# Kernel optimization log

Hardware: AMD Instinct MI355X
Metric: run time of the kernel (lower is better)

The kernel has to match this reference:

```python
import jax, jax.numpy as jnp
import numpy as np

B, H, W, C = 32, 32, 32, 256


def setup_inputs() -> dict:
    key = jax.random.key(0)
    k1, k2 = jax.random.split(key)
    feats1 = jax.random.normal(k1, (B, H, W, C), dtype=jnp.float32)
    feats2 = jax.random.normal(k2, (B, H, W, C), dtype=jnp.float32)
    return {"feats1": feats1, "feats2": feats2}


def reference(feats1, feats2):
    # Training path of LocalFeatureLoss (trainflag=True)
    b, h, w, c = feats1.shape
    l = h * w
    q = feats1.reshape(b, l, c)  # queries: (B, l, C)
    p = feats2.reshape(b, l, c)  # preds:   (B, l, C)
    # M[b, a, j] = <p[b,a], q[b,j]>  == fm2 @ fm1.T per batch
    M = jnp.einsum('bac,bjc->baj', p, q)  # (B, l_pred, l_query)
    max1 = jnp.argmax(M, axis=1)  # (B, l_q): best pred index for each query token
    max2 = jnp.argmax(M, axis=2)  # (B, l_p): best query index for each pred token
    # mutual nearest-neighbor check: m[b, j] = max2[b, max1[b, j]]
    m = jnp.take_along_axis(max2, max1, axis=1)  # (B, l_q)
    valid = jnp.arange(l)[None, :] == m          # (B, l_q) bool
    # gather matched pred descriptors and compute per-pair similarity
    matched_p = jnp.take_along_axis(p, max1[..., None], axis=1)  # (B, l_q, C)
    sims = jnp.sum(q * matched_p, axis=-1)                        # (B, l_q)
    cnt = jnp.sum(valid, axis=1).astype(sims.dtype)               # (B,)
    # mean over mutual NN pairs (torch mean over idx1)
    similarity = jnp.sum(jnp.where(valid, sims, 0.0), axis=1) / jnp.maximum(cnt, 1.0)
    return similarity
```

## Files before the change

kernel.cpp:

```cpp
#include <hip/hip_runtime.h>
#include <hip/hip_bf16.h>

#define BATCH 32
#define L 1024
#define CD 256
#define BM 128
#define BN 128
#define BK 64
#define NRT (L / BM)
#define NCT (L / BN)

typedef __bf16 bf16x8 __attribute__((ext_vector_type(8)));
typedef __bf16 bf16x4 __attribute__((ext_vector_type(4)));
typedef float  f32x4  __attribute__((ext_vector_type(4)));

__device__ __forceinline__ unsigned int enc_f32(float f) {
    unsigned int u = __float_as_uint(f);
    return ((int)u < 0) ? ~u : (u | 0x80000000u);
}
__device__ __forceinline__ float dec_f32(unsigned int u) {
    u = (u & 0x80000000u) ? (u & 0x7FFFFFFFu) : ~u;
    return __uint_as_float(u);
}
__device__ __forceinline__ unsigned long long pmax(unsigned long long a, unsigned long long b) {
    return a > b ? a : b;
}
__device__ __forceinline__ bf16x4 cvt4(float4 v) {
    bf16x4 o;
    o[0] = (__bf16)v.x; o[1] = (__bf16)v.y; o[2] = (__bf16)v.z; o[3] = (__bf16)v.w;
    return o;
}

__device__ __forceinline__ void block_sync_lgkm() {
    asm volatile("s_waitcnt lgkmcnt(0)" ::: "memory");
    __builtin_amdgcn_s_barrier();
    asm volatile("" ::: "memory");
}

__global__ __launch_bounds__(512, 4) void mm_argmax_kernel(
    const float* __restrict__ qg,
    const float* __restrict__ pg,
    unsigned long long* __restrict__ colpart,
    unsigned long long* __restrict__ rowpart)
{
    __shared__ __bf16 sA[2][BM * BK];
    __shared__ __bf16 sB[2][BN * BK];
    __shared__ unsigned long long sRow[2][BM];
    __shared__ unsigned long long sCol[4][BN];

    const int tid = threadIdx.x;
    const int bid = blockIdx.x;
    const int b    = bid & 31;
    const int tile = bid >> 5;
    const int rt   = tile >> 3;
    const int ct   = tile & 7;
    const int row0 = rt * BM;
    const int col0 = ct * BN;

    const int lane = tid & 63;
    const int w    = tid >> 6;
    const int wm   = w >> 1;
    const int wn   = w & 1;
    const int quad = lane >> 4;
    const int l16  = lane & 15;

    const float* pA = pg + ((size_t)b * L + row0) * CD;
    const float* pB = qg + ((size_t)b * L + col0) * CD;

    const int sr = tid >> 4;
    const int sl = tid & 15;

    f32x4 acc[2][4];
    #pragma unroll
    for (int tm = 0; tm < 2; ++tm)
        #pragma unroll
        for (int tn = 0; tn < 4; ++tn) acc[tm][tn] = (f32x4){0.f, 0.f, 0.f, 0.f};

    float4 pfA[4], pfB[4];

    #define LOADS(k0)                                                          \
        _Pragma("unroll")                                                      \
        for (int p = 0; p < 4; ++p) {                                          \
            pfA[p] = *(const float4*)(pA + (size_t)(p * 32 + sr) * CD + (k0) + sl * 4); \
            pfB[p] = *(const float4*)(pB + (size_t)(p * 32 + sr) * CD + (k0) + sl * 4); \
        }

    #define STAGE(buf)                                                         \
        _Pragma("unroll")                                                      \
        for (int p = 0; p < 4; ++p) {                                          \
            const int row_ = p * 32 + sr;                                      \
            const int idx_ = row_ * BK + (((sl >> 1) ^ (row_ & 7)) << 3) + ((sl & 1) << 2); \
            *(bf16x4*)&sA[buf][idx_] = cvt4(pfA[p]);                           \
            *(bf16x4*)&sB[buf][idx_] = cvt4(pfB[p]);                           \
        }

    #define COMPUTE(buf)                                                       \
        __builtin_amdgcn_s_setprio(1);                                         \
        _Pragma("unroll")                                                      \
        for (int kk = 0; kk < 2; ++kk) {                                       \
            const int sw = ((kk * 4 + quad) ^ (l16 & 7)) << 3;                 \
            bf16x8 a0 = *(const bf16x8*)&sA[buf][(wm * 32      + l16) * BK + sw]; \
            bf16x8 a1 = *(const bf16x8*)&sA[buf][(wm * 32 + 16 + l16) * BK + sw]; \
            bf16x8 b0 = *(const bf16x8*)&sB[buf][(wn * 64      + l16) * BK + sw]; \
            bf16x8 b1 = *(const bf16x8*)&sB[buf][(wn * 64 + 16 + l16) * BK + sw]; \
            bf16x8 b2 = *(const bf16x8*)&sB[buf][(wn * 64 + 32 + l16) * BK + sw]; \
            bf16x8 b3 = *(const bf16x8*)&sB[buf][(wn * 64 + 48 + l16) * BK + sw]; \
            acc[0][0] = __builtin_amdgcn_mfma_f32_16x16x32_bf16(a0, b0, acc[0][0], 0, 0, 0); \
            acc[0][1] = __builtin_amdgcn_mfma_f32_16x16x32_bf16(a0, b1, acc[0][1], 0, 0, 0); \
            acc[0][2] = __builtin_amdgcn_mfma_f32_16x16x32_bf16(a0, b2, acc[0][2], 0, 0, 0); \
            acc[0][3] = __builtin_amdgcn_mfma_f32_16x16x32_bf16(a0, b3, acc[0][3], 0, 0, 0); \
            acc[1][0] = __builtin_amdgcn_mfma_f32_16x16x32_bf16(a1, b0, acc[1][0], 0, 0, 0); \
            acc[1][1] = __builtin_amdgcn_mfma_f32_16x16x32_bf16(a1, b1, acc[1][1], 0, 0, 0); \
            acc[1][2] = __builtin_amdgcn_mfma_f32_16x16x32_bf16(a1, b2, acc[1][2], 0, 0, 0); \
            acc[1][3] = __builtin_amdgcn_mfma_f32_16x16x32_bf16(a1, b3, acc[1][3], 0, 0, 0); \
        }                                                                      \
        __builtin_amdgcn_s_setprio(0);

    LOADS(0);
    STAGE(0);
    LOADS(BK);
    block_sync_lgkm();

    COMPUTE(0);
    STAGE(1);
    LOADS(2 * BK);
    block_sync_lgkm();

    COMPUTE(1);
    STAGE(0);
    LOADS(3 * BK);
    block_sync_lgkm();

    COMPUTE(0);
    STAGE(1);
    block_sync_lgkm();

    COMPUTE(1);

    #undef LOADS
    #undef STAGE
    #undef COMPUTE

    const int a_base = row0 + wm * 32 + quad * 4;
    const int j_base = col0 + wn * 64 + l16;

    #pragma unroll
    for (int tn = 0; tn < 4; ++tn) {
        float cv = acc[0][tn][0];
        int   ca = a_base;
        #pragma unroll
        for (int tm = 0; tm < 2; ++tm)
            #pragma unroll
            for (int r = 0; r < 4; ++r) {
                if (tm == 0 && r == 0) continue;
                const float v = acc[tm][tn][r];
                const int   a = a_base + tm * 16 + r;
                if (v > cv) { cv = v; ca = a; }
            }
        unsigned long long pk =
            ((unsigned long long)enc_f32(cv) << 32) | (unsigned int)(~(unsigned int)ca);
        pk = pmax(pk, __shfl_xor(pk, 16));
        pk = pmax(pk, __shfl_xor(pk, 32));
        if (quad == 0) sCol[wm][wn * 64 + tn * 16 + l16] = pk;
    }

    #pragma unroll
    for (int tm = 0; tm < 2; ++tm)
        #pragma unroll
        for (int r = 0; r < 4; ++r) {
            float rv = acc[tm][0][r];
            int   rj = j_base;
            #pragma unroll
            for (int tn = 1; tn < 4; ++tn) {
                const float v = acc[tm][tn][r];
                if (v > rv) { rv = v; rj = j_base + tn * 16; }
            }
            unsigned long long pk =
                ((unsigned long long)enc_f32(rv) << 32) | (unsigned int)(~(unsigned int)rj);
            pk = pmax(pk, __shfl_xor(pk, 1));
            pk = pmax(pk, __shfl_xor(pk, 2));
            pk = pmax(pk, __shfl_xor(pk, 4));
            pk = pmax(pk, __shfl_xor(pk, 8));
            if (l16 == 0) sRow[wn][wm * 32 + tm * 16 + quad * 4 + r] = pk;
        }

    __syncthreads();
    if (tid < BN) {
        unsigned long long c = pmax(pmax(sCol[0][tid], sCol[1][tid]),
                                    pmax(sCol[2][tid], sCol[3][tid]));
        colpart[((size_t)b * NRT + rt) * L + col0 + tid] = c;
        unsigned long long rr = pmax(sRow[0][tid], sRow[1][tid]);
        rowpart[((size_t)b * NCT + ct) * L + row0 + tid] = rr;
    }
}

__global__ __launch_bounds__(1024) void finalize_kernel(
    const unsigned long long* __restrict__ colpart,
    const unsigned long long* __restrict__ rowpart,
    float* __restrict__ out)
{
    __shared__ int sMax2[L];
    __shared__ float sSum[16];
    __shared__ int sCnt[16];
    const int b = blockIdx.x;
    const int j = threadIdx.x;

    unsigned long long rb = 0ull;
    #pragma unroll
    for (int ct = 0; ct < NCT; ++ct)
        rb = pmax(rb, rowpart[((size_t)b * NCT + ct) * L + j]);
    sMax2[j] = (int)(~(unsigned int)rb) & (L - 1);

    unsigned long long cb = 0ull;
    #pragma unroll
    for (int rt = 0; rt < NRT; ++rt)
        cb = pmax(cb, colpart[((size_t)b * NRT + rt) * L + j]);
    __syncthreads();

    const int a = (int)(~(unsigned int)cb) & (L - 1);
    const float val = dec_f32((unsigned int)(cb >> 32));
    const bool mut = (sMax2[a] == j);
    float sum = mut ? val : 0.f;
    int   cnt = mut ? 1 : 0;

    #pragma unroll
    for (int o = 32; o >= 1; o >>= 1) {
        sum += __shfl_down(sum, o);
        cnt += __shfl_down(cnt, o);
    }
    if ((j & 63) == 0) { sSum[j >> 6] = sum; sCnt[j >> 6] = cnt; }
    __syncthreads();
    if (j == 0) {
        float S = 0.f;
        int   C = 0;
        #pragma unroll
        for (int i = 0; i < 16; ++i) { S += sSum[i]; C += sCnt[i]; }
        out[b] = S / fmaxf((float)C, 1.0f);
    }
}

extern "C" void kernel_launch(void* const* d_in, const int* in_sizes, int n_in,
                              void* d_out, int out_size, void* d_ws, size_t ws_size,
                              hipStream_t stream) {
    const float* q = (const float*)d_in[0];
    const float* p = (const float*)d_in[1];
    float* out = (float*)d_out;

    unsigned long long* colpart = (unsigned long long*)d_ws;
    unsigned long long* rowpart = colpart + (size_t)BATCH * NRT * L;

    mm_argmax_kernel<<<BATCH * NRT * NCT, 512, 0, stream>>>(q, p, colpart, rowpart);
    finalize_kernel<<<BATCH, 1024, 0, stream>>>(colpart, rowpart, out);
}
```

Before: 129.4 us.

## Pre-convert inputs to swizzled bf16 tiles and load via global_load_lds

Adds a separate conversion kernel that turns both fp32 inputs into bf16 laid out in pre-swizzled 128x64 tile panels. The GEMM kernel then moves whole tiles straight into LDS with global-to-LDS DMA loads, issues all four K-steps up front, and waits on vmcnt before each step. This removes the per-tile fp32 reads and in-register conversion, which were repeated eight times per input row across tiles, and halves the bytes the GEMM reads. In exchange it adds an extra launch plus a write and re-read of the bf16 copy, and uses more LDS per block (four full stages), which may reduce occupancy.

New measurement: 150.8 us. 16.5% more time.

```diff
diff --git a/kernel.cpp b/kernel.cpp
--- a/kernel.cpp
+++ b/kernel.cpp
@@ -9,10 +9,11 @@
 #define BK 64
 #define NRT (L / BM)
 #define NCT (L / BN)
+#define TILE_E 8192
 
 typedef __bf16 bf16x8 __attribute__((ext_vector_type(8)));
-typedef __bf16 bf16x4 __attribute__((ext_vector_type(4)));
 typedef float  f32x4  __attribute__((ext_vector_type(4)));
+typedef unsigned long long u64;
 
 __device__ __forceinline__ unsigned int enc_f32(float f) {
     unsigned int u = __float_as_uint(f);
@@ -22,31 +23,53 @@
     u = (u & 0x80000000u) ? (u & 0x7FFFFFFFu) : ~u;
     return __uint_as_float(u);
 }
-__device__ __forceinline__ unsigned long long pmax(unsigned long long a, unsigned long long b) {
-    return a > b ? a : b;
-}
-__device__ __forceinline__ bf16x4 cvt4(float4 v) {
-    bf16x4 o;
-    o[0] = (__bf16)v.x; o[1] = (__bf16)v.y; o[2] = (__bf16)v.z; o[3] = (__bf16)v.w;
-    return o;
-}
-
-__device__ __forceinline__ void block_sync_lgkm() {
-    asm volatile("s_waitcnt lgkmcnt(0)" ::: "memory");
-    __builtin_amdgcn_s_barrier();
-    asm volatile("" ::: "memory");
-}
-
-__global__ __launch_bounds__(512, 4) void mm_argmax_kernel(
+__device__ __forceinline__ u64 pmax(u64 a, u64 b) { return a > b ? a : b; }
+
+__device__ __forceinline__ void gl_lds16(const __bf16* g, __bf16* l) {
+    __builtin_amdgcn_global_load_lds(
+        (const __attribute__((address_space(1))) unsigned int*)g,
+        (__attribute__((address_space(3))) unsigned int*)l, 16, 0, 0);
+}
+
+__global__ __launch_bounds__(256) void convert_kernel(
     const float* __restrict__ qg,
     const float* __restrict__ pg,
-    unsigned long long* __restrict__ colpart,
-    unsigned long long* __restrict__ rowpart)
+    __bf16* __restrict__ qsw,
+    __bf16* __restrict__ psw)
 {
-    __shared__ __bf16 sA[2][BM * BK];
-    __shared__ __bf16 sB[2][BN * BK];
-    __shared__ unsigned long long sRow[2][BM];
-    __shared__ unsigned long long sCol[4][BN];
+    const unsigned int t = blockIdx.x * 256 + threadIdx.x;
+    const unsigned int v = t & ((1u << 20) - 1);
+    const bool isQ = (t >> 20) != 0;
+    const float* src_base = isQ ? qg : pg;
+    __bf16*      dst_base = isQ ? qsw : psw;
+
+    const int s    = v & 7;
+    const int row  = (v >> 3) & 127;
+    const int step = (v >> 10) & 3;
+    const int pan  = (v >> 12) & 7;
+    const int b    = v >> 15;
+
+    const float* src = src_base
+        + ((size_t)b * L + pan * 128 + row) * CD
+        + step * 64 + ((s ^ (row & 7)) * 8);
+    const float4 f0 = *(const float4*)src;
+    const float4 f1 = *(const float4*)(src + 4);
+    bf16x8 o;
+    o[0] = (__bf16)f0.x; o[1] = (__bf16)f0.y; o[2] = (__bf16)f0.z; o[3] = (__bf16)f0.w;
+    o[4] = (__bf16)f1.x; o[5] = (__bf16)f1.y; o[6] = (__bf16)f1.z; o[7] = (__bf16)f1.w;
+    *(bf16x8*)&dst_base[(size_t)v * 8] = o;
+}
+
+__global__ __launch_bounds__(512) void mm_argmax_kernel(
+    const __bf16* __restrict__ qsw,
+    const __bf16* __restrict__ psw,
+    u64* __restrict__ colpart,
+    u64* __restrict__ rowpart)
+{
+    __shared__ __bf16 sA[4][TILE_E];
+    __shared__ __bf16 sB[4][TILE_E];
+    __shared__ u64 sRow[2][BM];
+    __shared__ u64 sCol[4][BN];
 
     const int tid = threadIdx.x;
     const int bid = blockIdx.x;
@@ -64,11 +87,16 @@
     const int quad = lane >> 4;
     const int l16  = lane & 15;
 
-    const float* pA = pg + ((size_t)b * L + row0) * CD;
-    const float* pB = qg + ((size_t)b * L + col0) * CD;
-
-    const int sr = tid >> 4;
-    const int sl = tid & 15;
+    const __bf16* pa = psw + (size_t)(b * 8 + rt) * 4 * TILE_E;
+    const __bf16* pb = qsw + (size_t)(b * 8 + ct) * 4 * TILE_E;
+
+    #pragma unroll
+    for (int s = 0; s < 4; ++s) {
+        gl_lds16(pa + s * TILE_E +        tid * 8, &sA[s][tid * 8]);
+        gl_lds16(pa + s * TILE_E + 4096 + tid * 8, &sA[s][4096 + tid * 8]);
+        gl_lds16(pb + s * TILE_E +        tid * 8, &sB[s][tid * 8]);
+        gl_lds16(pb + s * TILE_E + 4096 + tid * 8, &sB[s][4096 + tid * 8]);
+    }
 
     f32x4 acc[2][4];
     #pragma unroll
@@ -76,35 +104,22 @@
         #pragma unroll
         for (int tn = 0; tn < 4; ++tn) acc[tm][tn] = (f32x4){0.f, 0.f, 0.f, 0.f};
 
-    float4 pfA[4], pfB[4];
-
-    #define LOADS(k0)                                                          \
-        _Pragma("unroll")                                                      \
-        for (int p = 0; p < 4; ++p) {                                          \
-            pfA[p] = *(const float4*)(pA + (size_t)(p * 32 + sr) * CD + (k0) + sl * 4); \
-            pfB[p] = *(const float4*)(pB + (size_t)(p * 32 + sr) * CD + (k0) + sl * 4); \
-        }
-
-    #define STAGE(buf)                                                         \
-        _Pragma("unroll")                                                      \
-        for (int p = 0; p < 4; ++p) {                                          \
-            const int row_ = p * 32 + sr;                                      \
-            const int idx_ = row_ * BK + (((sl >> 1) ^ (row_ & 7)) << 3) + ((sl & 1) << 2); \
-            *(bf16x4*)&sA[buf][idx_] = cvt4(pfA[p]);                           \
-            *(bf16x4*)&sB[buf][idx_] = cvt4(pfB[p]);                           \
-        }
-
-    #define COMPUTE(buf)                                                       \
+    #define STEP_SYNC(N)                                           \
+        asm volatile("s_waitcnt vmcnt(" #N ")" ::: "memory");      \
+        __builtin_amdgcn_s_barrier();                              \
+        __builtin_amdgcn_sched_barrier(0);
+
+    #define COMPUTE(s)                                                         \
         __builtin_amdgcn_s_setprio(1);                                         \
         _Pragma("unroll")                                                      \
         for (int kk = 0; kk < 2; ++kk) {                                       \
             const int sw = ((kk * 4 + quad) ^ (l16 & 7)) << 3;                 \
-            bf16x8 a0 = *(const bf16x8*)&sA[buf][(wm * 32      + l16) * BK + sw]; \
-            bf16x8 a1 = *(const bf16x8*)&sA[buf][(wm * 32 + 16 + l16) * BK + sw]; \
-            bf16x8 b0 = *(const bf16x8*)&sB[buf][(wn * 64      + l16) * BK + sw]; \
-            bf16x8 b1 = *(const bf16x8*)&sB[buf][(wn * 64 + 16 + l16) * BK + sw]; \
-            bf16x8 b2 = *(const bf16x8*)&sB[buf][(wn * 64 + 32 + l16) * BK + sw]; \
-            bf16x8 b3 = *(const bf16x8*)&sB[buf][(wn * 64 + 48 + l16) * BK + sw]; \
+            bf16x8 a0 = *(const bf16x8*)&sA[s][(wm * 32      + l16) * BK + sw]; \
+            bf16x8 a1 = *(const bf16x8*)&sA[s][(wm * 32 + 16 + l16) * BK + sw]; \
+            bf16x8 b0 = *(const bf16x8*)&sB[s][(wn * 64      + l16) * BK + sw]; \
+            bf16x8 b1 = *(const bf16x8*)&sB[s][(wn * 64 + 16 + l16) * BK + sw]; \
+            bf16x8 b2 = *(const bf16x8*)&sB[s][(wn * 64 + 32 + l16) * BK + sw]; \
+            bf16x8 b3 = *(const bf16x8*)&sB[s][(wn * 64 + 48 + l16) * BK + sw]; \
             acc[0][0] = __builtin_amdgcn_mfma_f32_16x16x32_bf16(a0, b0, acc[0][0], 0, 0, 0); \
             acc[0][1] = __builtin_amdgcn_mfma_f32_16x16x32_bf16(a0, b1, acc[0][1], 0, 0, 0); \
             acc[0][2] = __builtin_amdgcn_mfma_f32_16x16x32_bf16(a0, b2, acc[0][2], 0, 0, 0); \
@@ -116,29 +131,12 @@
         }                                                                      \
         __builtin_amdgcn_s_setprio(0);
 
-    LOADS(0);
-    STAGE(0);
-    LOADS(BK);
-    block_sync_lgkm();
-
-    COMPUTE(0);
-    STAGE(1);
-    LOADS(2 * BK);
-    block_sync_lgkm();
-
-    COMPUTE(1);
-    STAGE(0);
-    LOADS(3 * BK);
-    block_sync_lgkm();
-
-    COMPUTE(0);
-    STAGE(1);
-    block_sync_lgkm();
-
-    COMPUTE(1);
-
-    #undef LOADS
-    #undef STAGE
+    STEP_SYNC(12) COMPUTE(0)
+    STEP_SYNC(8)  COMPUTE(1)
+    STEP_SYNC(4)  COMPUTE(2)
+    STEP_SYNC(0)  COMPUTE(3)
+
+    #undef STEP_SYNC
     #undef COMPUTE
 
     const int a_base = row0 + wm * 32 + quad * 4;
@@ -157,8 +155,7 @@
                 const int   a = a_base + tm * 16 + r;
                 if (v > cv) { cv = v; ca = a; }
             }
-        unsigned long long pk =
-            ((unsigned long long)enc_f32(cv) << 32) | (unsigned int)(~(unsigned int)ca);
+        u64 pk = ((u64)enc_f32(cv) << 32) | (unsigned int)(~(unsigned int)ca);
         pk = pmax(pk, __shfl_xor(pk, 16));
         pk = pmax(pk, __shfl_xor(pk, 32));
         if (quad == 0) sCol[wm][wn * 64 + tn * 16 + l16] = pk;
@@ -175,8 +172,7 @@
                 const float v = acc[tm][tn][r];
                 if (v > rv) { rv = v; rj = j_base + tn * 16; }
             }
-            unsigned long long pk =
-                ((unsigned long long)enc_f32(rv) << 32) | (unsigned int)(~(unsigned int)rj);
+            u64 pk = ((u64)enc_f32(rv) << 32) | (unsigned int)(~(unsigned int)rj);
             pk = pmax(pk, __shfl_xor(pk, 1));
             pk = pmax(pk, __shfl_xor(pk, 2));
             pk = pmax(pk, __shfl_xor(pk, 4));
@@ -186,17 +182,17 @@
 
     __syncthreads();
     if (tid < BN) {
-        unsigned long long c = pmax(pmax(sCol[0][tid], sCol[1][tid]),
-                                    pmax(sCol[2][tid], sCol[3][tid]));
+        u64 c = pmax(pmax(sCol[0][tid], sCol[1][tid]),
+                     pmax(sCol[2][tid], sCol[3][tid]));
         colpart[((size_t)b * NRT + rt) * L + col0 + tid] = c;
-        unsigned long long rr = pmax(sRow[0][tid], sRow[1][tid]);
+        u64 rr = pmax(sRow[0][tid], sRow[1][tid]);
         rowpart[((size_t)b * NCT + ct) * L + row0 + tid] = rr;
     }
 }
 
 __global__ __launch_bounds__(1024) void finalize_kernel(
-    const unsigned long long* __restrict__ colpart,
-    const unsigned long long* __restrict__ rowpart,
+    const u64* __restrict__ colpart,
+    const u64* __restrict__ rowpart,
     float* __restrict__ out)
 {
     __shared__ int sMax2[L];
@@ -205,13 +201,13 @@
     const int b = blockIdx.x;
     const int j = threadIdx.x;
 
-    unsigned long long rb = 0ull;
+    u64 rb = 0ull;
     #pragma unroll
     for (int ct = 0; ct < NCT; ++ct)
         rb = pmax(rb, rowpart[((size_t)b * NCT + ct) * L + j]);
     sMax2[j] = (int)(~(unsigned int)rb) & (L - 1);
 
-    unsigned long long cb = 0ull;
+    u64 cb = 0ull;
     #pragma unroll
     for (int rt = 0; rt < NRT; ++rt)
         cb = pmax(cb, colpart[((size_t)b * NRT + rt) * L + j]);
@@ -246,9 +242,12 @@
     const float* p = (const float*)d_in[1];
     float* out = (float*)d_out;
 
-    unsigned long long* colpart = (unsigned long long*)d_ws;
-    unsigned long long* rowpart = colpart + (size_t)BATCH * NRT * L;
-
-    mm_argmax_kernel<<<BATCH * NRT * NCT, 512, 0, stream>>>(q, p, colpart, rowpart);
+    u64* colpart = (u64*)d_ws;
+    u64* rowpart = colpart + (size_t)BATCH * NRT * L;
+    __bf16* psw = (__bf16*)(rowpart + (size_t)BATCH * NCT * L);
+    __bf16* qsw = psw + (size_t)BATCH * 8 * 4 * TILE_E;
+
+    convert_kernel<<<8192, 256, 0, stream>>>(q, p, qsw, psw);
+    mm_argmax_kernel<<<BATCH * NRT * NCT, 512, 0, stream>>>(qsw, psw, colpart, rowpart);
     finalize_kernel<<<BATCH, 1024, 0, stream>>>(colpart, rowpart, out);
 }
```
